# Optimization experiments

Hardware: AMD Instinct MI355X
Metric: run time of the kernel (lower is better)

## Reference

```python
import jax, jax.numpy as jnp
import numpy as np

N = 8          # num merged RadialMLPs (experts)
D_IN = 64      # in_features
H = 128        # hidden_features
D_OUT = 64     # out_features
E = 100000     # num edges
LN_EPS = 1e-5


def setup_inputs() -> dict:
    key = jax.random.key(0)
    ks = jax.random.split(key, 12)
    s = lambda *shape: 0.05
    return {
        "x": jax.random.normal(ks[0], (E, D_IN), dtype=jnp.float32),
        # first layer concatenated across experts: [N*H, D_IN]
        "W1_cat": jax.random.normal(ks[1], (N * H, D_IN), dtype=jnp.float32) * 0.05,
        "b1_cat": jax.random.normal(ks[2], (N * H,), dtype=jnp.float32) * 0.05,
        "gamma1": jnp.ones((N, H), dtype=jnp.float32),
        "beta1": jnp.zeros((N, H), dtype=jnp.float32),
        "W2": jax.random.normal(ks[3], (N, H, H), dtype=jnp.float32) * 0.05,
        "b2": jax.random.normal(ks[4], (N, H), dtype=jnp.float32) * 0.05,
        "gamma2": jnp.ones((N, H), dtype=jnp.float32),
        "beta2": jnp.zeros((N, H), dtype=jnp.float32),
        "W3": jax.random.normal(ks[5], (N, D_OUT, H), dtype=jnp.float32) * 0.05,
        "b3": jax.random.normal(ks[6], (N, D_OUT), dtype=jnp.float32) * 0.05,
    }


def _layer_norm(h, gamma, beta):
    # h: [E, N, H]; gamma/beta: [N, H]; normalize over last dim (biased var)
    mu = jnp.mean(h, axis=-1, keepdims=True)
    var = jnp.mean(jnp.square(h - mu), axis=-1, keepdims=True)
    hn = (h - mu) * jax.lax.rsqrt(var + LN_EPS)
    return hn * gamma[None, :, :] + beta[None, :, :]


def reference(x, W1_cat, b1_cat, gamma1, beta1, W2, b2, gamma2, beta2, W3, b3):
    # Shared first GEMM: [E, D_IN] x [D_IN, N*H] -> [E, N, H]
    h = (x @ W1_cat.T + b1_cat).reshape(x.shape[0], N, H)
    h = jax.nn.silu(_layer_norm(h, gamma1, beta1))
    # Per-expert Linear 2, batched: W2 is [N, H_out, H_in]
    h = jnp.einsum("enh,nkh->enk", h, W2) + b2[None, :, :]
    h = jax.nn.silu(_layer_norm(h, gamma2, beta2))
    # Per-expert Linear 3: W3 is [N, D_OUT, H]
    out = jnp.einsum("enh,noh->eno", h, W3) + b3[None, :, :]
    # [N, E, D_OUT]: stack of the N per-expert outputs (original returns a list)
    return jnp.transpose(out, (1, 0, 2))
```

## Files before the change

kernel.cpp:

```cpp
#include <hip/hip_runtime.h>

#define NEXP 8
#define E_TOT 100000
#define EPB 128
#define NTILE 782
#define HSTR 136

typedef __bf16 bf16x8 __attribute__((ext_vector_type(8)));
typedef float f32x4 __attribute__((ext_vector_type(4)));
typedef unsigned short u16x8 __attribute__((ext_vector_type(8)));

union BF8 { u16x8 u; bf16x8 b; };
union BW  { __bf16 h; unsigned short u; };

__device__ __forceinline__ unsigned short f2bf(float f) {
  unsigned int u = __float_as_uint(f);
  u += 0x7fffu + ((u >> 16) & 1u);
  return (unsigned short)(u >> 16);
}

__device__ __forceinline__ bf16x8 fragld(const unsigned short* a, int off) {
  BF8 t;
  t.u = *(const u16x8*)(a + off);
  return t.b;
}

__device__ __forceinline__ bf16x8 frag_f32(const float* s) {
  float4 u0 = *(const float4*)s;
  float4 u1 = *(const float4*)(s + 4);
  BF8 t;
  t.u[0]=f2bf(u0.x); t.u[1]=f2bf(u0.y); t.u[2]=f2bf(u0.z); t.u[3]=f2bf(u0.w);
  t.u[4]=f2bf(u1.x); t.u[5]=f2bf(u1.y); t.u[6]=f2bf(u1.z); t.u[7]=f2bf(u1.w);
  return t.b;
}

__global__ void k_conv_w(const float* __restrict__ W1c, const float* __restrict__ W2p,
                         const float* __restrict__ W3p, unsigned short* __restrict__ wsW) {
  int gid = blockIdx.x * 256 + threadIdx.x;
  int n = gid >> 15, p = gid & 32767;
  int idx, frag, t, s, row;
  const float* base;
  int K;
  if (p < 8192)       { idx = p;         frag = idx >> 9; t = frag >> 1; s = frag & 1;
                        base = W1c + (size_t)n * 8192;  K = 64; }
  else if (p < 24576) { idx = p - 8192;  frag = idx >> 9; t = frag >> 2; s = frag & 3;
                        base = W2p + (size_t)n * 16384; K = 128; }
  else                { idx = p - 24576; frag = idx >> 9; t = frag >> 2; s = frag & 3;
                        base = W3p + (size_t)n * 8192;  K = 128; }
  int r = idx & 511, lane = r >> 3, j = r & 7;
  int l15 = lane & 15, gq = lane >> 4;
  row = (p < 24576) ? (8 * l15 + t) : (4 * l15 + t);
  wsW[gid] = f2bf(base[row * K + 32 * s + 8 * gq + j]);
}

__global__ void k_conv_x(const float* __restrict__ xg, unsigned short* __restrict__ xb) {
  int gid = blockIdx.x * 256 + threadIdx.x;
  const float* s = xg + (size_t)gid * 8;
  BF8 t;
  float4 a = *(const float4*)s, b = *(const float4*)(s + 4);
  t.u[0]=f2bf(a.x); t.u[1]=f2bf(a.y); t.u[2]=f2bf(a.z); t.u[3]=f2bf(a.w);
  t.u[4]=f2bf(b.x); t.u[5]=f2bf(b.y); t.u[6]=f2bf(b.z); t.u[7]=f2bf(b.w);
  *(u16x8*)(xb + (size_t)gid * 8) = t.u;
}

template <bool USEWS>
__global__ __launch_bounds__(256, 3) void k_main(
    const unsigned short* __restrict__ wsW, const unsigned short* __restrict__ xb,
    const float* __restrict__ xg,
    const float* __restrict__ W1c, const float* __restrict__ b1c,
    const float* __restrict__ g1p, const float* __restrict__ bt1p,
    const float* __restrict__ W2p, const float* __restrict__ b2p,
    const float* __restrict__ g2p, const float* __restrict__ bt2p,
    const float* __restrict__ W3p, const float* __restrict__ b3p,
    float* __restrict__ outp)
{
  __shared__ __attribute__((aligned(16))) unsigned short hs[EPB * HSTR];
  __shared__ __attribute__((aligned(16))) float prm[832];

  const int bid = blockIdx.x;
  const int g_  = (bid & 7) * NTILE + (bid >> 3);
  const int tile = g_ >> 3;
  const int n    = g_ & 7;
  const int e0   = tile * EPB;

  const int tid  = threadIdx.x;
  const int lane = tid & 63;
  const int wv   = tid >> 6;
  const int l15  = lane & 15;
  const int gq   = lane >> 4;
  const int wrow = wv * 32;

  for (int i = tid; i < 832; i += 256) {
    int grp = i >> 7, f = i & 127;
    float v;
    switch (grp) {
      case 0: v = b1c [n * 128 + f]; break;
      case 1: v = g1p [n * 128 + f]; break;
      case 2: v = bt1p[n * 128 + f]; break;
      case 3: v = b2p [n * 128 + f]; break;
      case 4: v = g2p [n * 128 + f]; break;
      case 5: v = bt2p[n * 128 + f]; break;
      default: v = b3p[n * 64 + f]; break;
    }
    prm[i] = v;
  }

  bf16x8 ax[2][2];
#pragma unroll
  for (int rt = 0; rt < 2; ++rt) {
    int e = e0 + wrow + 16 * rt + l15;
    if (e >= E_TOT) e = E_TOT - 1;
    if (USEWS) {
#pragma unroll
      for (int s = 0; s < 2; ++s)
        ax[rt][s] = fragld(xb, e * 64 + s * 32 + 8 * gq);
    } else {
#pragma unroll
      for (int s = 0; s < 2; ++s)
        ax[rt][s] = frag_f32(xg + (size_t)e * 64 + s * 32 + 8 * gq);
    }
  }

  const unsigned short* wf1 = wsW + (size_t)n * 32768;
  const unsigned short* wf2 = wf1 + 8192;
  const unsigned short* wf3 = wf1 + 24576;
  const float* W1n = W1c + (size_t)n * 8192;
  const float* W2n = W2p + (size_t)n * 16384;
  const float* W3n = W3p + (size_t)n * 8192;

  auto wfrag = [&](const unsigned short* wf, const float* Wn, int fidx, int row, int s, int K) {
    if (USEWS) return fragld(wf, (fidx << 9) + (lane << 3));
    return frag_f32(Wn + row * K + 32 * s + 8 * gq);
  };

  __syncthreads();

  f32x4 acc[2][8];

  auto ln_silu_store = [&](int pb) {
#pragma unroll
    for (int rt = 0; rt < 2; ++rt) {
      f32x4 sm4 = acc[rt][0];
      f32x4 sq4 = acc[rt][0] * acc[rt][0];
#pragma unroll
      for (int ct = 1; ct < 8; ++ct) {
        f32x4 v = acc[rt][ct];
        sm4 += v;
        sq4 += v * v;
      }
#pragma unroll
      for (int m = 1; m <= 8; m <<= 1) {
        f32x4 so, qo;
#pragma unroll
        for (int j = 0; j < 4; ++j) {
          so[j] = __shfl_xor(sm4[j], m);
          qo[j] = __shfl_xor(sq4[j], m);
        }
        sm4 += so;
        sq4 += qo;
      }
      f32x4 mu  = sm4 * (1.f / 128.f);
      f32x4 var = sq4 * (1.f / 128.f) - mu * mu;
      f32x4 rs;
#pragma unroll
      for (int j = 0; j < 4; ++j) rs[j] = __builtin_amdgcn_rsqf(var[j] + 1e-5f);
      f32x4 murs = mu * rs;
      float4 g01 = *(const float4*)&prm[pb + 128 + 8 * l15];
      float4 g23 = *(const float4*)&prm[pb + 128 + 8 * l15 + 4];
      float4 t01 = *(const float4*)&prm[pb + 256 + 8 * l15];
      float4 t23 = *(const float4*)&prm[pb + 256 + 8 * l15 + 4];
      const float* gv  = (const float*)&g01;
      const float* gv2 = (const float*)&g23;
      const float* bv  = (const float*)&t01;
      const float* bv2 = (const float*)&t23;
      unsigned short* hbase = hs + (wrow + 16 * rt + 4 * gq) * HSTR + 8 * l15;
#pragma unroll
      for (int j = 0; j < 4; ++j) {
        BF8 t8;
#pragma unroll
        for (int ct = 0; ct < 8; ++ct) {
          float g = (ct < 4) ? gv[ct] : gv2[ct - 4];
          float bb = (ct < 4) ? bv[ct] : bv2[ct - 4];
          float v = acc[rt][ct][j] * rs[j] - murs[j];
          v = v * g + bb;
          v = v * __builtin_amdgcn_rcpf(1.f + __expf(-v));
          BW bw; bw.h = (__bf16)v;
          t8.u[ct] = bw.u;
        }
        *(u16x8*)(hbase + j * HSTR) = t8.u;
      }
    }
  };

  {
    float4 b01 = *(const float4*)&prm[8 * l15];
    float4 b23 = *(const float4*)&prm[8 * l15 + 4];
    const float* bp  = (const float*)&b01;
    const float* bp2 = (const float*)&b23;
#pragma unroll
    for (int ct = 0; ct < 8; ++ct) {
      float bv = (ct < 4) ? bp[ct] : bp2[ct - 4];
      f32x4 b4 = {bv, bv, bv, bv};
      acc[0][ct] = b4;
      acc[1][ct] = b4;
    }
  }
#pragma unroll
  for (int s = 0; s < 2; ++s) {
#pragma unroll
    for (int ct = 0; ct < 8; ++ct) {
      bf16x8 b = wfrag(wf1, W1n, ct * 2 + s, 8 * l15 + ct, s, 64);
      acc[0][ct] = __builtin_amdgcn_mfma_f32_16x16x32_bf16(ax[0][s], b, acc[0][ct], 0, 0, 0);
      acc[1][ct] = __builtin_amdgcn_mfma_f32_16x16x32_bf16(ax[1][s], b, acc[1][ct], 0, 0, 0);
    }
  }
  ln_silu_store(0);

  const unsigned short* ha0 = hs + (wrow + l15) * HSTR + 8 * gq;
  const unsigned short* ha1 = hs + (wrow + 16 + l15) * HSTR + 8 * gq;
  {
    float4 b01 = *(const float4*)&prm[384 + 8 * l15];
    float4 b23 = *(const float4*)&prm[384 + 8 * l15 + 4];
    const float* bp  = (const float*)&b01;
    const float* bp2 = (const float*)&b23;
#pragma unroll
    for (int ct = 0; ct < 8; ++ct) {
      float bv = (ct < 4) ? bp[ct] : bp2[ct - 4];
      f32x4 b4 = {bv, bv, bv, bv};
      acc[0][ct] = b4;
      acc[1][ct] = b4;
    }
  }
#pragma unroll
  for (int ks = 0; ks < 4; ++ks) {
    bf16x8 a0 = fragld(ha0, ks * 32);
    bf16x8 a1 = fragld(ha1, ks * 32);
#pragma unroll
    for (int ct = 0; ct < 8; ++ct) {
      bf16x8 b = wfrag(wf2, W2n, ct * 4 + ks, 8 * l15 + ct, ks, 128);
      acc[0][ct] = __builtin_amdgcn_mfma_f32_16x16x32_bf16(a0, b, acc[0][ct], 0, 0, 0);
      acc[1][ct] = __builtin_amdgcn_mfma_f32_16x16x32_bf16(a1, b, acc[1][ct], 0, 0, 0);
    }
  }
  ln_silu_store(384);

  f32x4 a3[2][4];
  {
    float4 b34 = *(const float4*)&prm[768 + 4 * l15];
#pragma unroll
    for (int t = 0; t < 4; ++t) {
      float bv = ((const float*)&b34)[t];
      f32x4 b4 = {bv, bv, bv, bv};
      a3[0][t] = b4;
      a3[1][t] = b4;
    }
  }
#pragma unroll
  for (int ks = 0; ks < 4; ++ks) {
    bf16x8 a0 = fragld(ha0, ks * 32);
    bf16x8 a1 = fragld(ha1, ks * 32);
#pragma unroll
    for (int t = 0; t < 4; ++t) {
      bf16x8 b = wfrag(wf3, W3n, t * 4 + ks, 4 * l15 + t, ks, 128);
      a3[0][t] = __builtin_amdgcn_mfma_f32_16x16x32_bf16(a0, b, a3[0][t], 0, 0, 0);
      a3[1][t] = __builtin_amdgcn_mfma_f32_16x16x32_bf16(a1, b, a3[1][t], 0, 0, 0);
    }
  }

#pragma unroll
  for (int rt = 0; rt < 2; ++rt) {
#pragma unroll
    for (int j = 0; j < 4; ++j) {
      int e = e0 + wrow + 16 * rt + 4 * gq + j;
      if (e < E_TOT) {
        float4 o4;
        o4.x = a3[rt][0][j]; o4.y = a3[rt][1][j];
        o4.z = a3[rt][2][j]; o4.w = a3[rt][3][j];
        *(float4*)(outp + ((size_t)n * E_TOT + e) * 64 + 4 * l15) = o4;
      }
    }
  }
}

extern "C" void kernel_launch(void* const* d_in, const int* in_sizes, int n_in,
                              void* d_out, int out_size, void* d_ws, size_t ws_size,
                              hipStream_t stream) {
  (void)in_sizes; (void)n_in; (void)out_size;
  const float* xg   = (const float*)d_in[0];
  const float* W1c  = (const float*)d_in[1];
  const float* b1c  = (const float*)d_in[2];
  const float* g1p  = (const float*)d_in[3];
  const float* bt1p = (const float*)d_in[4];
  const float* W2p  = (const float*)d_in[5];
  const float* b2p  = (const float*)d_in[6];
  const float* g2p  = (const float*)d_in[7];
  const float* bt2p = (const float*)d_in[8];
  const float* W3p  = (const float*)d_in[9];
  const float* b3p  = (const float*)d_in[10];
  float* outp = (float*)d_out;

  const size_t WS_W = (size_t)NEXP * 32768 * sizeof(unsigned short);
  const size_t WS_X = (size_t)E_TOT * 64 * sizeof(unsigned short);
  const bool usews = ws_size >= WS_W + WS_X;

  dim3 grid(NEXP * NTILE, 1, 1);
  dim3 block(256, 1, 1);

  if (usews) {
    unsigned short* wsW = (unsigned short*)d_ws;
    unsigned short* xb  = wsW + (size_t)NEXP * 32768;
    k_conv_w<<<1024, 256, 0, stream>>>(W1c, W2p, W3p, wsW);
    k_conv_x<<<3125, 256, 0, stream>>>(xg, xb);
    k_main<true><<<grid, block, 0, stream>>>(wsW, xb, xg, W1c, b1c, g1p, bt1p,
                                             W2p, b2p, g2p, bt2p, W3p, b3p, outp);
  } else {
    k_main<false><<<grid, block, 0, stream>>>(nullptr, nullptr, xg, W1c, b1c, g1p, bt1p,
                                              W2p, b2p, g2p, bt2p, W3p, b3p, outp);
  }
}
```

Measured before the change: 141.2 us.

## Double edge tile per block to reuse weight fragments across four row tiles

Each block now covers 256 edges instead of 128, so every wave handles 64 rows (four 16-row MFMA tiles) and each loaded weight fragment feeds four MFMAs instead of two. This halves per-edge weight fragment traffic and the per-block parameter setup, at the cost of a larger LDS tile and twice the accumulator registers, so launch bounds drop to 2 blocks per CU. The layernorm affine step is also applied in vector form with gamma/beta loaded once per call, which should trim scalar work in the epilogue.

```diff
diff --git a/kernel.cpp b/kernel.cpp
--- a/kernel.cpp
+++ b/kernel.cpp
@@ -2,8 +2,8 @@
 
 #define NEXP 8
 #define E_TOT 100000
-#define EPB 128
-#define NTILE 782
+#define EPB 256
+#define NTILE 391
 #define HSTR 136
 
 typedef __bf16 bf16x8 __attribute__((ext_vector_type(8)));
@@ -64,7 +64,7 @@
 }
 
 template <bool USEWS>
-__global__ __launch_bounds__(256, 3) void k_main(
+__global__ __launch_bounds__(256, 2) void k_main(
     const unsigned short* __restrict__ wsW, const unsigned short* __restrict__ xb,
     const float* __restrict__ xg,
     const float* __restrict__ W1c, const float* __restrict__ b1c,
@@ -88,7 +88,7 @@
   const int wv   = tid >> 6;
   const int l15  = lane & 15;
   const int gq   = lane >> 4;
-  const int wrow = wv * 32;
+  const int wrow = wv * 64;
 
   for (int i = tid; i < 832; i += 256) {
     int grp = i >> 7, f = i & 127;
@@ -105,9 +105,9 @@
     prm[i] = v;
   }
 
-  bf16x8 ax[2][2];
-#pragma unroll
-  for (int rt = 0; rt < 2; ++rt) {
+  bf16x8 ax[4][2];
+#pragma unroll
+  for (int rt = 0; rt < 4; ++rt) {
     int e = e0 + wrow + 16 * rt + l15;
     if (e >= E_TOT) e = E_TOT - 1;
     if (USEWS) {
@@ -135,11 +135,19 @@
 
   __syncthreads();
 
-  f32x4 acc[2][8];
+  f32x4 acc[4][8];
 
   auto ln_silu_store = [&](int pb) {
-#pragma unroll
-    for (int rt = 0; rt < 2; ++rt) {
+    float4 g01 = *(const float4*)&prm[pb + 128 + 8 * l15];
+    float4 g23 = *(const float4*)&prm[pb + 128 + 8 * l15 + 4];
+    float4 t01 = *(const float4*)&prm[pb + 256 + 8 * l15];
+    float4 t23 = *(const float4*)&prm[pb + 256 + 8 * l15 + 4];
+    const float* gv  = (const float*)&g01;
+    const float* gv2 = (const float*)&g23;
+    const float* bv  = (const float*)&t01;
+    const float* bv2 = (const float*)&t23;
+#pragma unroll
+    for (int rt = 0; rt < 4; ++rt) {
       f32x4 sm4 = acc[rt][0];
       f32x4 sq4 = acc[rt][0] * acc[rt][0];
 #pragma unroll
@@ -165,24 +173,21 @@
 #pragma unroll
       for (int j = 0; j < 4; ++j) rs[j] = __builtin_amdgcn_rsqf(var[j] + 1e-5f);
       f32x4 murs = mu * rs;
-      float4 g01 = *(const float4*)&prm[pb + 128 + 8 * l15];
-      float4 g23 = *(const float4*)&prm[pb + 128 + 8 * l15 + 4];
-      float4 t01 = *(const float4*)&prm[pb + 256 + 8 * l15];
-      float4 t23 = *(const float4*)&prm[pb + 256 + 8 * l15 + 4];
-      const float* gv  = (const float*)&g01;
-      const float* gv2 = (const float*)&g23;
-      const float* bv  = (const float*)&t01;
-      const float* bv2 = (const float*)&t23;
+#pragma unroll
+      for (int ct = 0; ct < 8; ++ct) {
+        float g  = (ct < 4) ? gv[ct] : gv2[ct - 4];
+        float bb = (ct < 4) ? bv[ct] : bv2[ct - 4];
+        f32x4 g4 = {g, g, g, g};
+        f32x4 b4 = {bb, bb, bb, bb};
+        acc[rt][ct] = (acc[rt][ct] * rs - murs) * g4 + b4;
+      }
       unsigned short* hbase = hs + (wrow + 16 * rt + 4 * gq) * HSTR + 8 * l15;
 #pragma unroll
       for (int j = 0; j < 4; ++j) {
         BF8 t8;
 #pragma unroll
         for (int ct = 0; ct < 8; ++ct) {
-          float g = (ct < 4) ? gv[ct] : gv2[ct - 4];
-          float bb = (ct < 4) ? bv[ct] : bv2[ct - 4];
-          float v = acc[rt][ct][j] * rs[j] - murs[j];
-          v = v * g + bb;
+          float v = acc[rt][ct][j];
           v = v * __builtin_amdgcn_rcpf(1.f + __expf(-v));
           BW bw; bw.h = (__bf16)v;
           t8.u[ct] = bw.u;
@@ -199,10 +204,10 @@
     const float* bp2 = (const float*)&b23;
 #pragma unroll
     for (int ct = 0; ct < 8; ++ct) {
-      float bv = (ct < 4) ? bp[ct] : bp2[ct - 4];
-      f32x4 b4 = {bv, bv, bv, bv};
-      acc[0][ct] = b4;
-      acc[1][ct] = b4;
+      float bvv = (ct < 4) ? bp[ct] : bp2[ct - 4];
+      f32x4 b4 = {bvv, bvv, bvv, bvv};
+#pragma unroll
+      for (int rt = 0; rt < 4; ++rt) acc[rt][ct] = b4;
     }
   }
 #pragma unroll
@@ -210,14 +215,17 @@
 #pragma unroll
     for (int ct = 0; ct < 8; ++ct) {
       bf16x8 b = wfrag(wf1, W1n, ct * 2 + s, 8 * l15 + ct, s, 64);
-      acc[0][ct] = __builtin_amdgcn_mfma_f32_16x16x32_bf16(ax[0][s], b, acc[0][ct], 0, 0, 0);
-      acc[1][ct] = __builtin_amdgcn_mfma_f32_16x16x32_bf16(ax[1][s], b, acc[1][ct], 0, 0, 0);
+#pragma unroll
+      for (int rt = 0; rt < 4; ++rt)
+        acc[rt][ct] = __builtin_amdgcn_mfma_f32_16x16x32_bf16(ax[rt][s], b, acc[rt][ct], 0, 0, 0);
     }
   }
   ln_silu_store(0);
 
-  const unsigned short* ha0 = hs + (wrow + l15) * HSTR + 8 * gq;
-  const unsigned short* ha1 = hs + (wrow + 16 + l15) * HSTR + 8 * gq;
+  const unsigned short* ha[4];
+#pragma unroll
+  for (int rt = 0; rt < 4; ++rt)
+    ha[rt] = hs + (wrow + 16 * rt + l15) * HSTR + 8 * gq;
   {
     float4 b01 = *(const float4*)&prm[384 + 8 * l15];
     float4 b23 = *(const float4*)&prm[384 + 8 * l15 + 4];
@@ -225,57 +233,65 @@
     const float* bp2 = (const float*)&b23;
 #pragma unroll
     for (int ct = 0; ct < 8; ++ct) {
-      float bv = (ct < 4) ? bp[ct] : bp2[ct - 4];
-      f32x4 b4 = {bv, bv, bv, bv};
-      acc[0][ct] = b4;
-      acc[1][ct] = b4;
+      float bvv = (ct < 4) ? bp[ct] : bp2[ct - 4];
+      f32x4 b4 = {bvv, bvv, bvv, bvv};
+#pragma unroll
+      for (int rt = 0; rt < 4; ++rt) acc[rt][ct] = b4;
     }
   }
 #pragma unroll
   for (int ks = 0; ks < 4; ++ks) {
-    bf16x8 a0 = fragld(ha0, ks * 32);
-    bf16x8 a1 = fragld(ha1, ks * 32);
+    bf16x8 a0 = fragld(ha[0], ks * 32);
+    bf16x8 a1 = fragld(ha[1], ks * 32);
+    bf16x8 a2 = fragld(ha[2], ks * 32);
+    bf16x8 a3f = fragld(ha[3], ks * 32);
 #pragma unroll
     for (int ct = 0; ct < 8; ++ct) {
       bf16x8 b = wfrag(wf2, W2n, ct * 4 + ks, 8 * l15 + ct, ks, 128);
-      acc[0][ct] = __builtin_amdgcn_mfma_f32_16x16x32_bf16(a0, b, acc[0][ct], 0, 0, 0);
-      acc[1][ct] = __builtin_amdgcn_mfma_f32_16x16x32_bf16(a1, b, acc[1][ct], 0, 0, 0);
+      acc[0][ct] = __builtin_amdgcn_mfma_f32_16x16x32_bf16(a0,  b, acc[0][ct], 0, 0, 0);
+      acc[1][ct] = __builtin_amdgcn_mfma_f32_16x16x32_bf16(a1,  b, acc[1][ct], 0, 0, 0);
+      acc[2][ct] = __builtin_amdgcn_mfma_f32_16x16x32_bf16(a2,  b, acc[2][ct], 0, 0, 0);
+      acc[3][ct] = __builtin_amdgcn_mfma_f32_16x16x32_bf16(a3f, b, acc[3][ct], 0, 0, 0);
     }
   }
   ln_silu_store(384);
 
-  f32x4 a3[2][4];
+  f32x4 o3[4][4];
   {
     float4 b34 = *(const float4*)&prm[768 + 4 * l15];
 #pragma unroll
     for (int t = 0; t < 4; ++t) {
-      float bv = ((const float*)&b34)[t];
-      f32x4 b4 = {bv, bv, bv, bv};
-      a3[0][t] = b4;
-      a3[1][t] = b4;
+      float bvv = ((const float*)&b34)[t];
+      f32x4 b4 = {bvv, bvv, bvv, bvv};
+#pragma unroll
+      for (int rt = 0; rt < 4; ++rt) o3[rt][t] = b4;
     }
   }
 #pragma unroll
   for (int ks = 0; ks < 4; ++ks) {
-    bf16x8 a0 = fragld(ha0, ks * 32);
-    bf16x8 a1 = fragld(ha1, ks * 32);
+    bf16x8 a0 = fragld(ha[0], ks * 32);
+    bf16x8 a1 = fragld(ha[1], ks * 32);
+    bf16x8 a2 = fragld(ha[2], ks * 32);
+    bf16x8 a3f = fragld(ha[3], ks * 32);
 #pragma unroll
     for (int t = 0; t < 4; ++t) {
       bf16x8 b = wfrag(wf3, W3n, t * 4 + ks, 4 * l15 + t, ks, 128);
-      a3[0][t] = __builtin_amdgcn_mfma_f32_16x16x32_bf16(a0, b, a3[0][t], 0, 0, 0);
-      a3[1][t] = __builtin_amdgcn_mfma_f32_16x16x32_bf16(a1, b, a3[1][t], 0, 0, 0);
-    }
-  }
-
-#pragma unroll
-  for (int rt = 0; rt < 2; ++rt) {
+      o3[0][t] = __builtin_amdgcn_mfma_f32_16x16x32_bf16(a0,  b, o3[0][t], 0, 0, 0);
+      o3[1][t] = __builtin_amdgcn_mfma_f32_16x16x32_bf16(a1,  b, o3[1][t], 0, 0, 0);
+      o3[2][t] = __builtin_amdgcn_mfma_f32_16x16x32_bf16(a2,  b, o3[2][t], 0, 0, 0);
+      o3[3][t] = __builtin_amdgcn_mfma_f32_16x16x32_bf16(a3f, b, o3[3][t], 0, 0, 0);
+    }
+  }
+
+#pragma unroll
+  for (int rt = 0; rt < 4; ++rt) {
 #pragma unroll
     for (int j = 0; j < 4; ++j) {
       int e = e0 + wrow + 16 * rt + 4 * gq + j;
       if (e < E_TOT) {
         float4 o4;
-        o4.x = a3[rt][0][j]; o4.y = a3[rt][1][j];
-        o4.z = a3[rt][2][j]; o4.w = a3[rt][3][j];
+        o4.x = o3[rt][0][j]; o4.y = o3[rt][1][j];
+        o4.z = o3[rt][2][j]; o4.w = o3[rt][3][j];
         *(float4*)(outp + ((size_t)n * E_TOT + e) * 64 + 4 * l15) = o4;
       }
     }
```

New measurement: 164.7 us. +16.6%, slower.
